# Optimization experiments

Measured on AMD Instinct MI355X. Metric: run time of the kernel, lower is better.

Reference implementation:

```python
import jax, jax.numpy as jnp
import numpy as np

H = 256; W = 256; TS = 4
EYE_Z = 2.732                     # nr camera position (0,0,2.732)
FOCAL = float(1.0 / np.tan(np.deg2rad(15.0)))  # 30-deg viewing angle
BIG = 1e10
EPS = 1e-8


def _render(vertices, faces, textures, angle):
    """Differentiable z-buffer rasterizer with trilinear per-face texture cubes.
    Ambient light = 1.0, directional = 0.0, so shading == sampled texture color."""
    v = vertices[0]                    # [V,3]
    f = faces[0]                       # [F,3] int
    tex = jnp.tanh(textures)[0]        # [F,TS,TS,TS,3]
    P = H * W

    # camera orbit: rotate mesh about y by angle (fraction of full turn)
    th = angle[0] * (2.0 * jnp.pi)
    c, s = jnp.cos(th), jnp.sin(th)
    x, y, z = v[:, 0], v[:, 1], v[:, 2]
    xr = c * x + s * z
    zr = -s * x + c * z
    depth = EYE_Z - zr                 # camera at (0,0,EYE_Z) looking down -z
    px = FOCAL * xr / depth
    py = FOCAL * y / depth

    fx = px[f]; fy = py[f]; fd = depth[f]      # [F,3]
    ax, bx, cx = fx[:, 0], fx[:, 1], fx[:, 2]
    ay, by, cy = fy[:, 0], fy[:, 1], fy[:, 2]

    # pixel centers in NDC [-1,1]
    xs = (jnp.arange(W) + 0.5) / W * 2.0 - 1.0
    ys = 1.0 - (jnp.arange(H) + 0.5) / H * 2.0
    gy, gx = jnp.meshgrid(ys, xs, indexing='ij')
    pxp = gx.reshape(-1)[:, None]      # [P,1]
    pyp = gy.reshape(-1)[:, None]

    area = (bx - ax) * (cy - ay) - (by - ay) * (cx - ax)
    valid = jnp.abs(area) > EPS
    denom = jnp.where(valid, area, 1.0)

    def edge(x0, y0, x1, y1):
        # normalized edge function -> barycentric weight, shape [P,F]
        return ((x1 - x0) * (pyp - y0) - (y1 - y0) * (pxp - x0)) / denom

    w0 = edge(bx, by, cx, cy)
    w1 = edge(cx, cy, ax, ay)
    w2 = 1.0 - w0 - w1
    inside = (w0 >= 0) & (w1 >= 0) & (w2 >= 0) & valid[None, :]

    zpix = w0 * fd[:, 0] + w1 * fd[:, 1] + w2 * fd[:, 2]   # interpolated depth
    zbuf = jnp.where(inside & (zpix > EPS), zpix, BIG)
    fidx = jnp.argmin(zbuf, axis=1)                        # [P] winning face
    hit = jnp.take_along_axis(zbuf, fidx[:, None], 1)[:, 0] < 0.5 * BIG

    w0s = jnp.take_along_axis(w0, fidx[:, None], 1)[:, 0]
    w1s = jnp.take_along_axis(w1, fidx[:, None], 1)[:, 0]
    pw = jnp.stack([w0s, w1s, 1.0 - w0s - w1s], axis=-1)   # [P,3] barycentric

    # trilinear sample of the per-face TSxTSxTS texture cube at barycentric coords
    u = jnp.clip(pw, 0.0, 1.0) * (TS - 1)
    i0 = jnp.clip(jnp.floor(u), 0, TS - 2).astype(jnp.int32)
    fr = u - i0
    texp = tex[fidx].reshape(P, TS * TS * TS, 3)           # [P,64,3]
    col = jnp.zeros((P, 3), dtype=textures.dtype)
    for a in (0, 1):
        for b in (0, 1):
            for cc in (0, 1):
                idxf = (i0[:, 0] + a) * TS * TS + (i0[:, 1] + b) * TS + (i0[:, 2] + cc)
                wc = (jnp.where(a, fr[:, 0], 1.0 - fr[:, 0])
                      * jnp.where(b, fr[:, 1], 1.0 - fr[:, 1])
                      * jnp.where(cc, fr[:, 2], 1.0 - fr[:, 2]))
                col = col + wc[:, None] * jnp.take_along_axis(texp, idxf[:, None, None], axis=1)[:, 0, :]
    col = jnp.where(hit[:, None], col, 0.0)                # black background
    return col.T.reshape(1, 3, H, W)


def setup_inputs():
    key = jax.random.key(0)
    k1, k2, k3, k4, k5 = jax.random.split(key, 5)
    V, F = 322, 640
    vertices = 0.4 * jax.random.normal(k1, (1, V, 3), dtype=jnp.float32)
    faces = jax.random.randint(k2, (1, F, 3), 0, V, dtype=jnp.int32)
    textures = 0.5 * jax.random.normal(k3, (1, F, TS, TS, TS, 3), dtype=jnp.float32)
    image_ref = jax.random.uniform(k4, (1, 3, H, W), dtype=jnp.float32)
    angle = jax.random.uniform(k5, (1,), dtype=jnp.float32)
    return {"vertices": vertices, "faces": faces, "textures": textures,
            "image_ref": image_ref, "angle": angle}


def reference(vertices, faces, textures, image_ref, angle):
    image = _render(vertices, faces, textures, angle)
    return jnp.sum((image - image_ref) ** 2)
```

## Files before the change

kernel.cpp:

```cpp
#include <hip/hip_runtime.h>
#include <math.h>

#define NH 256
#define NW 256
#define NP (NH*NW)
#define NV 322
#define NF 640
#define EYE_Z 2.732f
#define BIGF 1.0e10f
#define EPSF 1.0e-8f
#define FOCALF 3.7320508075688776f
#define TILE_W 16
#define TILE_H 8
#define NTX (NW/TILE_W)
#define NTY (NH/TILE_H)
#define NBLK (NTX*NTY)
#define CULL_PAD 1e-5f


__global__ void texprep_kernel(const float* __restrict__ textures,
                               float4* __restrict__ texPad)
{
    int e = blockIdx.x * 256 + threadIdx.x;
    float v = tanhf(textures[e]);
    int fidx = e / 192;
    int r = e - fidx * 192;
    int t = r / 3;
    int ch = r - t * 3;
    ((float*)&texPad[fidx * 64 + t])[ch] = v;
}

__global__ __launch_bounds__(256, 2) void fused_kernel(
    const float* __restrict__ vertices,
    const int* __restrict__ faces,
    const float* __restrict__ angle,
    const float4* __restrict__ texPad,
    const float* __restrict__ ref,
    float* __restrict__ partials)
{
    __shared__ float4 pv[NV];
    __shared__ float4 list[NF * 3];
    __shared__ int wcnt[4];
    __shared__ float candZ[4][128];
    __shared__ int   candF[4][128];
    __shared__ float psum[2];

    int tid = threadIdx.x;
    int wave = tid >> 6;
    int lane = tid & 63;

    float th = angle[0] * 6.283185307179586f;
    float cth = cosf(th), sth = sinf(th);
    for (int t = tid; t < NV; t += 256) {
        float x = vertices[t * 3 + 0];
        float y = vertices[t * 3 + 1];
        float z = vertices[t * 3 + 2];
        float xr = cth * x + sth * z;
        float zr = -sth * x + cth * z;
        float depth = EYE_Z - zr;
        pv[t] = make_float4(FOCALF * xr / depth, FOCALF * y / depth, depth, 0.f);
    }
    __syncthreads();

    int tc = blockIdx.x & (NTX - 1);
    int tr = blockIdx.x >> 4;
    float x0 = ((float)(tc * TILE_W) + 0.5f) * (1.f / 128.f) - 1.f;
    float x1 = ((float)(tc * TILE_W + TILE_W - 1) + 0.5f) * (1.f / 128.f) - 1.f;
    float y1 = 1.f - ((float)(tr * TILE_H) + 0.5f) * (1.f / 128.f);
    float y0 = 1.f - ((float)(tr * TILE_H + TILE_H - 1) + 0.5f) * (1.f / 128.f);

    int nfl = 0;
    for (int rd = 0; rd < 3; ++rd) {
        int f = rd * 256 + tid;
        bool accept = false;
        float4 e0, e1, e2;
        if (f < NF) {
            int i0 = faces[f * 3 + 0], i1 = faces[f * 3 + 1], i2 = faces[f * 3 + 2];
            float4 pa = pv[i0], pb = pv[i1], pc = pv[i2];
            float area = (pb.x - pa.x) * (pc.y - pa.y) - (pb.y - pa.y) * (pc.x - pa.x);
            if (fabsf(area) > EPSF) {
                float xmn = fminf(fminf(pa.x, pb.x), pc.x);
                float xmx = fmaxf(fmaxf(pa.x, pb.x), pc.x);
                float ymn = fminf(fminf(pa.y, pb.y), pc.y);
                float ymx = fmaxf(fmaxf(pa.y, pb.y), pc.y);
                if (xmx >= x0 - CULL_PAD && xmn <= x1 + CULL_PAD &&
                    ymx >= y0 - CULL_PAD && ymn <= y1 + CULL_PAD) {
                    float inv = 1.0f / area;
                    float A0 = -(pc.y - pb.y) * inv;
                    float B0 =  (pc.x - pb.x) * inv;
                    float C0 =  (pb.x * (pc.y - pb.y) - pb.y * (pc.x - pb.x)) * inv;
                    float A1 = -(pa.y - pc.y) * inv;
                    float B1 =  (pa.x - pc.x) * inv;
                    float C1 =  (pc.x * (pa.y - pc.y) - pc.y * (pa.x - pc.x)) * inv;
                    float A2 = -(A0 + A1), B2 = -(B0 + B1), C2 = 1.f - C0 - C1;
                    float m0 = C0 + fmaxf(A0 * x0, A0 * x1) + fmaxf(B0 * y0, B0 * y1);
                    float m1 = C1 + fmaxf(A1 * x0, A1 * x1) + fmaxf(B1 * y0, B1 * y1);
                    float m2 = C2 + fmaxf(A2 * x0, A2 * x1) + fmaxf(B2 * y0, B2 * y1);
                    if (m0 >= -CULL_PAD && m1 >= -CULL_PAD && m2 >= -CULL_PAD) {
                        accept = true;
                        float zA = pa.z - pc.z, zB = pb.z - pc.z;
                        float Az = zA * A0 + zB * A1;
                        float Bz = zA * B0 + zB * B1;
                        float Cz = zA * C0 + zB * C1 + pc.z;
                        e0 = make_float4(A0, B0, C0, A1);
                        e1 = make_float4(B1, C1, Az, Bz);
                        e2 = make_float4(Cz, __int_as_float(f), 0.f, 0.f);
                    }
                }
            }
        }
        unsigned long long m = __ballot(accept);
        if (lane == 0) wcnt[wave] = (int)__popcll(m);
        __syncthreads();
        int base = nfl;
        if (wave > 0) base += wcnt[0];
        if (wave > 1) base += wcnt[1];
        if (wave > 2) base += wcnt[2];
        int pos = base + (int)__popcll(m & ((1ULL << lane) - 1ULL));
        if (accept) {
            list[pos * 3 + 0] = e0;
            list[pos * 3 + 1] = e1;
            list[pos * 3 + 2] = e2;
        }
        nfl += wcnt[0] + wcnt[1] + wcnt[2] + wcnt[3];
        __syncthreads();
    }

    int nflu = __builtin_amdgcn_readfirstlane(nfl);
    int c0 = (nflu * wave) >> 2;
    int c1 = (nflu * (wave + 1)) >> 2;
    int colp = tc * TILE_W + (lane & 15);
    int rowp = tr * TILE_H + (lane >> 4);
    float px  = ((float)colp + 0.5f) * (1.f / 128.f) - 1.f;
    float pya = 1.f - ((float)rowp + 0.5f) * (1.f / 128.f);
    const float DPY = -0.03125f;

    float zmin0 = BIGF, zmin1 = BIGF;
    int best0 = 0, best1 = 0;
    for (int i = c0; i < c1; ++i) {
        float4 d0 = list[i * 3 + 0];
        float4 d1 = list[i * 3 + 1];
        float czv = list[i * 3 + 2].x;
        float w0a = fmaf(d0.x, px, fmaf(d0.y, pya, d0.z));
        float w1a = fmaf(d0.w, px, fmaf(d1.x, pya, d1.y));
        float za  = fmaf(d1.z, px, fmaf(d1.w, pya, czv));
        float w0b = fmaf(DPY, d0.y, w0a);
        float w1b = fmaf(DPY, d1.x, w1a);
        float zb  = fmaf(DPY, d1.w, za);
        float mna = fminf(fminf(w0a, w1a), 1.f - w0a - w1a);
        float mnb = fminf(fminf(w0b, w1b), 1.f - w0b - w1b);
        bool oka = (mna >= 0.f) && (za < zmin0);
        bool okb = (mnb >= 0.f) && (zb < zmin1);
        zmin0 = oka ? za : zmin0;  best0 = oka ? i : best0;
        zmin1 = okb ? zb : zmin1;  best1 = okb ? i : best1;
    }
    candZ[wave][lane] = zmin0;      candF[wave][lane] = best0;
    candZ[wave][lane + 64] = zmin1; candF[wave][lane + 64] = best1;
    __syncthreads();

    if (wave < 2) {
        int sq = wave * 64 + lane;
        float zb = candZ[0][sq];
        int fb = candF[0][sq];
#pragma unroll
        for (int k = 1; k < 4; ++k) {
            float zk = candZ[k][sq];
            int fk = candF[k][sq];
            bool t = zk < zb;
            zb = t ? zk : zb;
            fb = t ? fk : fb;
        }
        bool hit = zb < 0.5f * BIGF;

        int colq = tc * TILE_W + (sq & 15);
        int rowq = tr * TILE_H + (sq >> 4);
        int p = rowq * 256 + colq;
        float pxq = ((float)colq + 0.5f) * (1.f / 128.f) - 1.f;
        float pyq = 1.f - ((float)rowq + 0.5f) * (1.f / 128.f);

        float4 d0 = list[fb * 3 + 0];
        float4 d1 = list[fb * 3 + 1];
        int forig = __float_as_int(list[fb * 3 + 2].y);
        int ftex = hit ? forig : 0;

        float bw0 = fmaf(d0.x, pxq, fmaf(d0.y, pyq, d0.z));
        float bw1 = fmaf(d0.w, pxq, fmaf(d1.x, pyq, d1.y));
        float pw2 = 1.f - bw0 - bw1;
        float u0 = fminf(fmaxf(bw0, 0.f), 1.f) * 3.f;
        float u1 = fminf(fmaxf(bw1, 0.f), 1.f) * 3.f;
        float u2 = fminf(fmaxf(pw2, 0.f), 1.f) * 3.f;
        int i0 = min(max((int)floorf(u0), 0), 2);
        int i1 = min(max((int)floorf(u1), 0), 2);
        int i2 = min(max((int)floorf(u2), 0), 2);
        float fr0 = u0 - (float)i0;
        float fr1 = u1 - (float)i1;
        float fr2 = u2 - (float)i2;

        const float4* tb = texPad + ftex * 64;
        float cr = 0.f, cg = 0.f, cb = 0.f;
#pragma unroll
        for (int a = 0; a < 2; a++) {
#pragma unroll
            for (int bbi = 0; bbi < 2; bbi++) {
#pragma unroll
                for (int cc = 0; cc < 2; cc++) {
                    int idx = (i0 + a) * 16 + (i1 + bbi) * 4 + (i2 + cc);
                    float w = (a ? fr0 : 1.f - fr0) * (bbi ? fr1 : 1.f - fr1) * (cc ? fr2 : 1.f - fr2);
                    float4 t = tb[idx];
                    cr = fmaf(w, t.x, cr);
                    cg = fmaf(w, t.y, cg);
                    cb = fmaf(w, t.z, cb);
                }
            }
        }
        if (!hit) { cr = 0.f; cg = 0.f; cb = 0.f; }

        float e0v = cr - ref[p];
        float e1v = cg - ref[NP + p];
        float e2v = cb - ref[2 * NP + p];
        float e = fmaf(e0v, e0v, fmaf(e1v, e1v, e2v * e2v));
#pragma unroll
        for (int off = 32; off > 0; off >>= 1) e += __shfl_down(e, off, 64);
        if (lane == 0) psum[wave] = e;
    }
    __syncthreads();
    if (tid == 0) partials[blockIdx.x] = psum[0] + psum[1];
}

__global__ __launch_bounds__(256) void reduce_kernel(
    const float* __restrict__ partials, float* __restrict__ out)
{
    __shared__ float wsum[4];
    int tid = threadIdx.x;
    float s = partials[tid] + partials[tid + 256];
#pragma unroll
    for (int off = 32; off > 0; off >>= 1) s += __shfl_down(s, off, 64);
    int lane = tid & 63;
    int wid = tid >> 6;
    if (lane == 0) wsum[wid] = s;
    __syncthreads();
    if (tid == 0) out[0] = wsum[0] + wsum[1] + wsum[2] + wsum[3];
}

extern "C" void kernel_launch(void* const* d_in, const int* in_sizes, int n_in,
                              void* d_out, int out_size, void* d_ws, size_t ws_size,
                              hipStream_t stream) {
    const float* vertices = (const float*)d_in[0];
    const int* faces = (const int*)d_in[1];
    const float* textures = (const float*)d_in[2];
    const float* image_ref = (const float*)d_in[3];
    const float* angle = (const float*)d_in[4];
    float* out = (float*)d_out;

    float4* texPad = (float4*)d_ws;
    float* partials = (float*)((char*)d_ws + 655360);

    texprep_kernel<<<480, 256, 0, stream>>>(textures, texPad);
    fused_kernel<<<NBLK, 256, 0, stream>>>(vertices, faces, angle,
                                           texPad, image_ref, partials);
    reduce_kernel<<<1, 256, 0, stream>>>(partials, out);
}
```

Measured before the change: 75.67 us.

## Precompute per-face edge coefficients and tile bounds once; drop reduce kernel via atomics

Moves vertex projection and per-face edge/depth coefficient setup out of every tile block into a single prep kernel, which also emits a packed integer tile-range bounding box per face. Tile blocks then cull faces with integer compares and load precomputed coefficients instead of recomputing them. The separate reduce kernel is removed: each tile block atomically adds its partial sum into the output, which prep zeroes. This saves one launch and redundant per-block setup, at the cost of extra global reads and non-deterministic float summation order.

```diff
diff --git a/kernel.cpp b/kernel.cpp
--- a/kernel.cpp
+++ b/kernel.cpp
@@ -16,29 +16,111 @@
 #define NTY (NH/TILE_H)
 #define NBLK (NTX*NTY)
 #define CULL_PAD 1e-5f
-
-
-__global__ void texprep_kernel(const float* __restrict__ textures,
-                               float4* __restrict__ texPad)
+#define PADP 0.01f
+
+
+__global__ void prep_kernel(const float* __restrict__ vertices,
+                            const int* __restrict__ faces,
+                            const float* __restrict__ textures,
+                            const float* __restrict__ angle,
+                            float4* __restrict__ texPad,
+                            float4* __restrict__ fA,
+                            float4* __restrict__ fB,
+                            float* __restrict__ czArr,
+                            int* __restrict__ bboxI,
+                            float* __restrict__ out)
 {
-    int e = blockIdx.x * 256 + threadIdx.x;
-    float v = tanhf(textures[e]);
-    int fidx = e / 192;
-    int r = e - fidx * 192;
-    int t = r / 3;
-    int ch = r - t * 3;
-    ((float*)&texPad[fidx * 64 + t])[ch] = v;
+    int b = blockIdx.x;
+    int tid = threadIdx.x;
+    if (b < 480) {
+        int e = b * 256 + tid;
+        float v = tanhf(textures[e]);
+        int fidx = e / 192;
+        int r = e - fidx * 192;
+        int t = r / 3;
+        int ch = r - t * 3;
+        ((float*)&texPad[fidx * 64 + t])[ch] = v;
+    } else if (b < 483) {
+        int j = (b - 480) * 256 + tid;
+        if (j < NF) {
+            float th = angle[0] * 6.283185307179586f;
+            float cth = cosf(th), sth = sinf(th);
+            float vx[3], vy[3], vd[3];
+#pragma unroll
+            for (int k = 0; k < 3; k++) {
+                int vi = faces[j * 3 + k];
+                float x = vertices[vi * 3 + 0];
+                float y = vertices[vi * 3 + 1];
+                float z = vertices[vi * 3 + 2];
+                float xr = cth * x + sth * z;
+                float zr = -sth * x + cth * z;
+                float depth = EYE_Z - zr;
+                vx[k] = FOCALF * xr / depth;
+                vy[k] = FOCALF * y / depth;
+                vd[k] = depth;
+            }
+            float ax = vx[0], ay = vy[0], bx = vx[1], by = vy[1], cx = vx[2], cy = vy[2];
+            float area = (bx - ax) * (cy - ay) - (by - ay) * (cx - ax);
+            float4 a4, b4;
+            float Cz = 0.f;
+            int packed = 0x00FF00FF;
+            if (fabsf(area) > EPSF) {
+                float inv = 1.0f / area;
+                float A0 = -(cy - by) * inv;
+                float B0 =  (cx - bx) * inv;
+                float C0 =  (bx * (cy - by) - by * (cx - bx)) * inv;
+                float A1 = -(ay - cy) * inv;
+                float B1 =  (ax - cx) * inv;
+                float C1 =  (cx * (ay - cy) - cy * (ax - cx)) * inv;
+                float zA = vd[0] - vd[2];
+                float zB = vd[1] - vd[2];
+                float Az = zA * A0 + zB * A1;
+                float Bz = zA * B0 + zB * B1;
+                Cz = zA * C0 + zB * C1 + vd[2];
+                a4 = make_float4(A0, B0, C0, A1);
+                b4 = make_float4(B1, C1, Az, Bz);
+                float xmn = fminf(fminf(ax, bx), cx);
+                float xmx = fmaxf(fmaxf(ax, bx), cx);
+                float ymn = fminf(fminf(ay, by), cy);
+                float ymx = fmaxf(fmaxf(ay, by), cy);
+                float xmn_px = (xmn + 1.f) * 128.f - 0.5f;
+                float xmx_px = (xmx + 1.f) * 128.f - 0.5f;
+                float rmn_px = (1.f - ymx) * 128.f - 0.5f;
+                float rmx_px = (1.f - ymn) * 128.f - 0.5f;
+                int txmin = (int)ceilf((xmn_px - PADP - (float)(TILE_W - 1)) / (float)TILE_W);
+                int txmax = (int)floorf((xmx_px + PADP) / (float)TILE_W);
+                int trmin = (int)ceilf((rmn_px - PADP - (float)(TILE_H - 1)) / (float)TILE_H);
+                int trmax = (int)floorf((rmx_px + PADP) / (float)TILE_H);
+                txmin = max(txmin, 0); txmax = min(txmax, NTX - 1);
+                trmin = max(trmin, 0); trmax = min(trmax, NTY - 1);
+                if (txmax < txmin || trmax < trmin) {
+                    packed = 0x00FF00FF;
+                } else {
+                    packed = txmin | (txmax << 8) | (trmin << 16) | (trmax << 24);
+                }
+            } else {
+                a4 = make_float4(0.f, 0.f, -1.f, 0.f);
+                b4 = make_float4(0.f, 0.f, 0.f, 0.f);
+            }
+            fA[j] = a4;
+            fB[j] = b4;
+            czArr[j] = Cz;
+            bboxI[j] = packed;
+        }
+    } else {
+        if (tid == 0) out[0] = 0.0f;
+    }
 }
 
 __global__ __launch_bounds__(256, 2) void fused_kernel(
-    const float* __restrict__ vertices,
-    const int* __restrict__ faces,
-    const float* __restrict__ angle,
+    const float4* __restrict__ fA,
+    const float4* __restrict__ fB,
+    const float* __restrict__ czArr,
+    const int* __restrict__ bboxI,
     const float4* __restrict__ texPad,
     const float* __restrict__ ref,
-    float* __restrict__ partials)
+    float* __restrict__ out)
 {
-    __shared__ float4 pv[NV];
     __shared__ float4 list[NF * 3];
     __shared__ int wcnt[4];
     __shared__ float candZ[4][128];
@@ -48,19 +130,6 @@
     int tid = threadIdx.x;
     int wave = tid >> 6;
     int lane = tid & 63;
-
-    float th = angle[0] * 6.283185307179586f;
-    float cth = cosf(th), sth = sinf(th);
-    for (int t = tid; t < NV; t += 256) {
-        float x = vertices[t * 3 + 0];
-        float y = vertices[t * 3 + 1];
-        float z = vertices[t * 3 + 2];
-        float xr = cth * x + sth * z;
-        float zr = -sth * x + cth * z;
-        float depth = EYE_Z - zr;
-        pv[t] = make_float4(FOCALF * xr / depth, FOCALF * y / depth, depth, 0.f);
-    }
-    __syncthreads();
 
     int tc = blockIdx.x & (NTX - 1);
     int tr = blockIdx.x >> 4;
@@ -73,39 +142,25 @@
     for (int rd = 0; rd < 3; ++rd) {
         int f = rd * 256 + tid;
         bool accept = false;
-        float4 e0, e1, e2;
+        float4 e0v, e1v, e2v;
         if (f < NF) {
-            int i0 = faces[f * 3 + 0], i1 = faces[f * 3 + 1], i2 = faces[f * 3 + 2];
-            float4 pa = pv[i0], pb = pv[i1], pc = pv[i2];
-            float area = (pb.x - pa.x) * (pc.y - pa.y) - (pb.y - pa.y) * (pc.x - pa.x);
-            if (fabsf(area) > EPSF) {
-                float xmn = fminf(fminf(pa.x, pb.x), pc.x);
-                float xmx = fmaxf(fmaxf(pa.x, pb.x), pc.x);
-                float ymn = fminf(fminf(pa.y, pb.y), pc.y);
-                float ymx = fmaxf(fmaxf(pa.y, pb.y), pc.y);
-                if (xmx >= x0 - CULL_PAD && xmn <= x1 + CULL_PAD &&
-                    ymx >= y0 - CULL_PAD && ymn <= y1 + CULL_PAD) {
-                    float inv = 1.0f / area;
-                    float A0 = -(pc.y - pb.y) * inv;
-                    float B0 =  (pc.x - pb.x) * inv;
-                    float C0 =  (pb.x * (pc.y - pb.y) - pb.y * (pc.x - pb.x)) * inv;
-                    float A1 = -(pa.y - pc.y) * inv;
-                    float B1 =  (pa.x - pc.x) * inv;
-                    float C1 =  (pc.x * (pa.y - pc.y) - pc.y * (pa.x - pc.x)) * inv;
-                    float A2 = -(A0 + A1), B2 = -(B0 + B1), C2 = 1.f - C0 - C1;
-                    float m0 = C0 + fmaxf(A0 * x0, A0 * x1) + fmaxf(B0 * y0, B0 * y1);
-                    float m1 = C1 + fmaxf(A1 * x0, A1 * x1) + fmaxf(B1 * y0, B1 * y1);
-                    float m2 = C2 + fmaxf(A2 * x0, A2 * x1) + fmaxf(B2 * y0, B2 * y1);
-                    if (m0 >= -CULL_PAD && m1 >= -CULL_PAD && m2 >= -CULL_PAD) {
-                        accept = true;
-                        float zA = pa.z - pc.z, zB = pb.z - pc.z;
-                        float Az = zA * A0 + zB * A1;
-                        float Bz = zA * B0 + zB * B1;
-                        float Cz = zA * C0 + zB * C1 + pc.z;
-                        e0 = make_float4(A0, B0, C0, A1);
-                        e1 = make_float4(B1, C1, Az, Bz);
-                        e2 = make_float4(Cz, __int_as_float(f), 0.f, 0.f);
-                    }
+            int bbp = bboxI[f];
+            int t0 = bbp & 255, t1 = (bbp >> 8) & 255;
+            int r0 = (bbp >> 16) & 255, r1 = (bbp >> 24) & 255;
+            if (tc >= t0 && tc <= t1 && tr >= r0 && tr <= r1) {
+                float4 a4 = fA[f];
+                float4 b4 = fB[f];
+                float A0 = a4.x, B0 = a4.y, C0 = a4.z, A1 = a4.w;
+                float B1 = b4.x, C1 = b4.y;
+                float A2 = -(A0 + A1), B2 = -(B0 + B1), C2 = 1.f - C0 - C1;
+                float m0 = C0 + fmaxf(A0 * x0, A0 * x1) + fmaxf(B0 * y0, B0 * y1);
+                float m1 = C1 + fmaxf(A1 * x0, A1 * x1) + fmaxf(B1 * y0, B1 * y1);
+                float m2 = C2 + fmaxf(A2 * x0, A2 * x1) + fmaxf(B2 * y0, B2 * y1);
+                if (m0 >= -CULL_PAD && m1 >= -CULL_PAD && m2 >= -CULL_PAD) {
+                    accept = true;
+                    e0v = a4;
+                    e1v = b4;
+                    e2v = make_float4(czArr[f], __int_as_float(f), 0.f, 0.f);
                 }
             }
         }
@@ -118,9 +173,9 @@
         if (wave > 2) base += wcnt[2];
         int pos = base + (int)__popcll(m & ((1ULL << lane) - 1ULL));
         if (accept) {
-            list[pos * 3 + 0] = e0;
-            list[pos * 3 + 1] = e1;
-            list[pos * 3 + 2] = e2;
+            list[pos * 3 + 0] = e0v;
+            list[pos * 3 + 1] = e1v;
+            list[pos * 3 + 2] = e2v;
         }
         nfl += wcnt[0] + wcnt[1] + wcnt[2] + wcnt[3];
         __syncthreads();
@@ -215,31 +270,16 @@
         }
         if (!hit) { cr = 0.f; cg = 0.f; cb = 0.f; }
 
-        float e0v = cr - ref[p];
-        float e1v = cg - ref[NP + p];
-        float e2v = cb - ref[2 * NP + p];
-        float e = fmaf(e0v, e0v, fmaf(e1v, e1v, e2v * e2v));
+        float e0e = cr - ref[p];
+        float e1e = cg - ref[NP + p];
+        float e2e = cb - ref[2 * NP + p];
+        float e = fmaf(e0e, e0e, fmaf(e1e, e1e, e2e * e2e));
 #pragma unroll
         for (int off = 32; off > 0; off >>= 1) e += __shfl_down(e, off, 64);
         if (lane == 0) psum[wave] = e;
     }
     __syncthreads();
-    if (tid == 0) partials[blockIdx.x] = psum[0] + psum[1];
-}
-
-__global__ __launch_bounds__(256) void reduce_kernel(
-    const float* __restrict__ partials, float* __restrict__ out)
-{
-    __shared__ float wsum[4];
-    int tid = threadIdx.x;
-    float s = partials[tid] + partials[tid + 256];
-#pragma unroll
-    for (int off = 32; off > 0; off >>= 1) s += __shfl_down(s, off, 64);
-    int lane = tid & 63;
-    int wid = tid >> 6;
-    if (lane == 0) wsum[wid] = s;
-    __syncthreads();
-    if (tid == 0) out[0] = wsum[0] + wsum[1] + wsum[2] + wsum[3];
+    if (tid == 0) atomicAdd(out, psum[0] + psum[1]);
 }
 
 extern "C" void kernel_launch(void* const* d_in, const int* in_sizes, int n_in,
@@ -252,11 +292,15 @@
     const float* angle = (const float*)d_in[4];
     float* out = (float*)d_out;
 
-    float4* texPad = (float4*)d_ws;
-    float* partials = (float*)((char*)d_ws + 655360);
-
-    texprep_kernel<<<480, 256, 0, stream>>>(textures, texPad);
-    fused_kernel<<<NBLK, 256, 0, stream>>>(vertices, faces, angle,
-                                           texPad, image_ref, partials);
-    reduce_kernel<<<1, 256, 0, stream>>>(partials, out);
+    char* ws = (char*)d_ws;
+    float4* texPad = (float4*)(ws);
+    float4* fAp    = (float4*)(ws + 655360);
+    float4* fBp    = (float4*)(ws + 665600);
+    float*  czArr  = (float*)(ws + 675840);
+    int*    bboxI  = (int*)(ws + 678400);
+
+    prep_kernel<<<484, 256, 0, stream>>>(vertices, faces, textures, angle,
+                                         texPad, fAp, fBp, czArr, bboxI, out);
+    fused_kernel<<<NBLK, 256, 0, stream>>>(fAp, fBp, czArr, bboxI,
+                                           texPad, image_ref, out);
 }
```

Result: faster. 73.64 us (-2.7%).
